# Optimization experiments

Hardware: AMD Instinct MI355X
Metric: run time of the kernel (lower is better)

Reference implementation:

```python
import jax, jax.numpy as jnp
import numpy as np

EMBED = 1024
HEADS = 16
HEAD_DIM = EMBED // HEADS
SCALE = HEAD_DIM ** -0.5


def setup_inputs() -> dict:
    key = jax.random.key(0)
    ks = jax.random.split(key, 9)
    B, N = 2, 2048
    std = EMBED ** -0.5
    return {
        "query": jax.random.normal(ks[0], (B, N, EMBED), jnp.float32),
        "key": jax.random.normal(ks[1], (B, N, EMBED), jnp.float32),
        "value": jax.random.normal(ks[2], (B, N, EMBED), jnp.float32),
        # torch nn.Linear weights are [out, in]; y = x @ W.T + b
        "Wq": jax.random.normal(ks[3], (EMBED, EMBED), jnp.float32) * std,
        "bq": jax.random.normal(ks[4], (EMBED,), jnp.float32) * 0.01,
        "Wk": jax.random.normal(ks[5], (EMBED, EMBED), jnp.float32) * std,
        "bk": jax.random.normal(ks[6], (EMBED,), jnp.float32) * 0.01,
        "Wv": jax.random.normal(ks[7], (EMBED, EMBED), jnp.float32) * std,
        "bv": jax.random.normal(ks[8], (EMBED,), jnp.float32) * 0.01,
    }


def reference(query, key, value, Wq, bq, Wk, bk, Wv, bv):
    B, NQ, _ = query.shape
    NK = key.shape[1]
    q = query @ Wq.T + bq  # [B, NQ, E]
    k = key @ Wk.T + bk    # [B, NK, E]
    v = value @ Wv.T + bv  # [B, NK, E]
    # split heads -> [B, H, N, Dh]
    q = q.reshape(B, NQ, HEADS, HEAD_DIM).transpose(0, 2, 1, 3)
    k = k.reshape(B, NK, HEADS, HEAD_DIM).transpose(0, 2, 1, 3)
    v = v.reshape(B, NK, HEADS, HEAD_DIM).transpose(0, 2, 1, 3)
    attn = jnp.einsum("bhqd,bhkd->bhqk", q, k) * SCALE  # [B, H, NQ, NK]
    attn = jax.nn.softmax(attn, axis=-1)
    out = jnp.einsum("bhqk,bhkd->bhqd", attn, v)  # [B, H, NQ, Dh]
    out = out.transpose(0, 2, 1, 3).reshape(B, NQ, EMBED)
    # o_proj is Identity (odim == embed_dim, o_proj=False); dropout is 0 (eval)
    return out
```

## Files before the change

kernel.cpp:

```cpp
#include <hip/hip_runtime.h>

#define EMB 1024
#define NSEQ 2048
#define NBATCH 2
#define NHEAD 16
#define DHEAD 64
#define QSCALE 0.18033688011112042f

typedef float f32x4 __attribute__((ext_vector_type(4)));
typedef short s16x8 __attribute__((ext_vector_type(8)));
typedef short s16x4 __attribute__((ext_vector_type(4)));

__device__ __forceinline__ short bf16r(float f) {
    unsigned u = __float_as_uint(f);
    u += 0x7fffu + ((u >> 16) & 1u);
    return (short)(u >> 16);
}

__device__ __forceinline__ unsigned pkbf(float a, float b) {
#if defined(__has_builtin) && __has_builtin(__builtin_amdgcn_cvt_pk_bf16_f32)
    auto r = __builtin_amdgcn_cvt_pk_bf16_f32(a, b);
    unsigned u;
    __builtin_memcpy(&u, &r, 4);
    return u;
#else
    return ((unsigned)bf16r(a) & 0xffffu) | ((unsigned)bf16r(b) << 16);
#endif
}

__device__ __forceinline__ float fexp2(float x) {
#if defined(__has_builtin) && __has_builtin(__builtin_amdgcn_exp2f)
    return __builtin_amdgcn_exp2f(x);
#else
    return exp2f(x);
#endif
}

__global__ __launch_bounds__(256) void proj_kernel(
    const float* __restrict__ Xq, const float* __restrict__ Xk, const float* __restrict__ Xv,
    const float* __restrict__ Wq, const float* __restrict__ Wk, const float* __restrict__ Wv,
    const float* __restrict__ bq, const float* __restrict__ bk, const float* __restrict__ bv,
    short* __restrict__ Oq, short* __restrict__ Ok, short* __restrict__ Ov)
{
    const int z = blockIdx.z;
    const float* X    = (z == 0) ? Xq : (z == 1) ? Xk : Xv;
    const float* W    = (z == 0) ? Wq : (z == 1) ? Wk : Wv;
    const float* bias = (z == 0) ? bq : (z == 1) ? bk : bv;
    short* Out        = (z == 0) ? Oq : (z == 1) ? Ok : Ov;
    const float osc   = (z == 0) ? QSCALE : 1.0f;

    const int n0 = blockIdx.x * 128;
    const int m0 = blockIdx.y * 128;

    __shared__ __align__(16) short As[128][40];
    __shared__ __align__(16) short Bs[128][40];

    const int t    = threadIdx.x;
    const int lane = t & 63;
    const int wave = t >> 6;
    const int r    = lane & 15;
    const int quad = lane >> 4;
    const int wm   = (wave >> 1) * 64;
    const int wn   = (wave & 1) * 64;

    const int srow = t >> 1;
    const int scol = (t & 1) << 4;

    f32x4 acc[4][4];
#pragma unroll
    for (int i = 0; i < 4; ++i)
#pragma unroll
        for (int j = 0; j < 4; ++j)
#pragma unroll
            for (int v = 0; v < 4; ++v) acc[i][j][v] = 0.f;

    for (int k0 = 0; k0 < EMB; k0 += 32) {
        const float4* xp = (const float4*)(X + (size_t)(m0 + srow) * EMB + k0 + scol);
        const float4* wp = (const float4*)(W + (size_t)(n0 + srow) * EMB + k0 + scol);
        float4 x0 = xp[0], x1 = xp[1], x2 = xp[2], x3 = xp[3];
        float4 w0 = wp[0], w1 = wp[1], w2 = wp[2], w3 = wp[3];
        uint4 a0 = { pkbf(x0.x, x0.y), pkbf(x0.z, x0.w), pkbf(x1.x, x1.y), pkbf(x1.z, x1.w) };
        uint4 a1 = { pkbf(x2.x, x2.y), pkbf(x2.z, x2.w), pkbf(x3.x, x3.y), pkbf(x3.z, x3.w) };
        uint4 b0 = { pkbf(w0.x, w0.y), pkbf(w0.z, w0.w), pkbf(w1.x, w1.y), pkbf(w1.z, w1.w) };
        uint4 b1 = { pkbf(w2.x, w2.y), pkbf(w2.z, w2.w), pkbf(w3.x, w3.y), pkbf(w3.z, w3.w) };
        *(uint4*)&As[srow][scol]     = a0;
        *(uint4*)&As[srow][scol + 8] = a1;
        *(uint4*)&Bs[srow][scol]     = b0;
        *(uint4*)&Bs[srow][scol + 8] = b1;
        __syncthreads();

        s16x8 af[4], bf[4];
#pragma unroll
        for (int i = 0; i < 4; ++i) af[i] = *(const s16x8*)&As[wm + i * 16 + r][quad * 8];
#pragma unroll
        for (int j = 0; j < 4; ++j) bf[j] = *(const s16x8*)&Bs[wn + j * 16 + r][quad * 8];
#pragma unroll
        for (int i = 0; i < 4; ++i)
#pragma unroll
            for (int j = 0; j < 4; ++j)
                acc[i][j] = __builtin_amdgcn_mfma_f32_16x16x32_bf16(af[i], bf[j], acc[i][j], 0, 0, 0);
        __syncthreads();
    }

#pragma unroll
    for (int j = 0; j < 4; ++j) {
        const int gn = n0 + wn + j * 16 + r;
        const float bv_ = bias[gn];
#pragma unroll
        for (int i = 0; i < 4; ++i)
#pragma unroll
            for (int reg = 0; reg < 4; ++reg) {
                const int gm = m0 + wm + i * 16 + quad * 4 + reg;
                Out[(size_t)gm * EMB + gn] = bf16r((acc[i][j][reg] + bv_) * osc);
            }
    }
}

__global__ __launch_bounds__(256) void vtrans_kernel(
    const short* __restrict__ Vp, short* __restrict__ VT)
{
    const int n0 = blockIdx.x * 64;
    const int h  = blockIdx.y;
    const int b  = blockIdx.z;
    __shared__ __align__(16) short L[64][72];

    const int t  = threadIdx.x;
    const int rr = t >> 2;
    const int cc = (t & 3) * 16;

    const short* src = Vp + (size_t)(b * NSEQ + n0 + rr) * EMB + h * DHEAD + cc;
    s16x8 a = *(const s16x8*)src;
    s16x8 c = *(const s16x8*)(src + 8);
    *(s16x8*)&L[rr][cc]     = a;
    *(s16x8*)&L[rr][cc + 8] = c;
    __syncthreads();

    const int d  = t >> 2;
    const int c4 = (t & 3) * 16;
    short vals[16];
#pragma unroll
    for (int i = 0; i < 16; ++i) vals[i] = L[c4 + i][d];
    short* dst = VT + ((size_t)(b * NHEAD + h) * DHEAD + d) * NSEQ + n0 + c4;
    *(s16x8*)dst       = *(s16x8*)&vals[0];
    *(s16x8*)(dst + 8) = *(s16x8*)&vals[8];
}

__global__ __launch_bounds__(256, 2) void attn2_kernel(
    const short* __restrict__ Qp, const short* __restrict__ Kp,
    const short* __restrict__ VT, float* __restrict__ Out)
{
    const int qblk = blockIdx.x * 128;
    const int h    = blockIdx.y;
    const int b    = blockIdx.z;

    __shared__ __align__(16) short Ks[64][72];
    __shared__ __align__(16) short Vs[64][72];
    __shared__ __align__(16) float fbuf[4][16][68];

    const int t    = threadIdx.x;
    const int lane = t & 63;
    const int w    = t >> 6;
    const int r    = lane & 15;
    const int quad = lane >> 4;

    const size_t rowbase = (size_t)b * NSEQ;
    const int colbase    = h * DHEAD;

    s16x8 qf[2][2];
#pragma unroll
    for (int qs = 0; qs < 2; ++qs)
#pragma unroll
        for (int ks = 0; ks < 2; ++ks)
            qf[qs][ks] = *(const s16x8*)(Qp + (rowbase + qblk + w * 32 + qs * 16 + r) * EMB
                                          + colbase + ks * 32 + quad * 8);

    f32x4 accO[2][4];
    float lsum[2] = {0.f, 0.f};
#pragma unroll
    for (int qs = 0; qs < 2; ++qs)
#pragma unroll
        for (int dt = 0; dt < 4; ++dt)
#pragma unroll
            for (int v = 0; v < 4; ++v) accO[qs][dt][v] = 0.f;

    const int srow = t >> 2;
    const int scol = (t & 3) << 4;

    const short* Kbase = Kp + (rowbase + srow) * EMB + colbase + scol;
    const short* Vbase = VT + ((size_t)(b * NHEAD + h) * DHEAD + srow) * NSEQ + scol;

    for (int kt = 0; kt < 32; ++kt) {
        const short* Ksrc = Kbase + (size_t)(kt * 64) * EMB;
        const short* Vsrc = Vbase + kt * 64;
        s16x8 k0 = *(const s16x8*)Ksrc, k1 = *(const s16x8*)(Ksrc + 8);
        s16x8 v0 = *(const s16x8*)Vsrc, v1 = *(const s16x8*)(Vsrc + 8);
        *(s16x8*)&Ks[srow][scol]     = k0;
        *(s16x8*)&Ks[srow][scol + 8] = k1;
        *(s16x8*)&Vs[srow][scol]     = v0;
        *(s16x8*)&Vs[srow][scol + 8] = v1;
        __syncthreads();

        s16x8 kf[4][2];
#pragma unroll
        for (int jt = 0; jt < 4; ++jt)
#pragma unroll
            for (int ks = 0; ks < 2; ++ks)
                kf[jt][ks] = *(const s16x8*)&Ks[jt * 16 + r][ks * 32 + quad * 8];

        s16x8 vf[4][2];
#pragma unroll
        for (int dt = 0; dt < 4; ++dt)
#pragma unroll
            for (int s = 0; s < 2; ++s) {
                s16x4 lo = *(const s16x4*)&Vs[dt * 16 + r][s * 32 + quad * 4];
                s16x4 hi = *(const s16x4*)&Vs[dt * 16 + r][s * 32 + 16 + quad * 4];
                vf[dt][s] = __builtin_shufflevector(lo, hi, 0, 1, 2, 3, 4, 5, 6, 7);
            }

        s16x8 pf[2][2];
#pragma unroll
        for (int qs = 0; qs < 2; ++qs) {
            f32x4 sacc[4];
#pragma unroll
            for (int jt = 0; jt < 4; ++jt) {
#pragma unroll
                for (int v = 0; v < 4; ++v) sacc[jt][v] = 0.f;
#pragma unroll
                for (int ks = 0; ks < 2; ++ks)
                    sacc[jt] = __builtin_amdgcn_mfma_f32_16x16x32_bf16(kf[jt][ks], qf[qs][ks], sacc[jt], 0, 0, 0);
            }
            float p[4][4];
#pragma unroll
            for (int jt = 0; jt < 4; ++jt)
#pragma unroll
                for (int reg = 0; reg < 4; ++reg) {
                    p[jt][reg] = fexp2(sacc[jt][reg]);
                    lsum[qs] += p[jt][reg];
                }
#pragma unroll
            for (int s = 0; s < 2; ++s) {
                uint4 uu = { pkbf(p[2 * s][0],     p[2 * s][1]),
                             pkbf(p[2 * s][2],     p[2 * s][3]),
                             pkbf(p[2 * s + 1][0], p[2 * s + 1][1]),
                             pkbf(p[2 * s + 1][2], p[2 * s + 1][3]) };
                __builtin_memcpy(&pf[qs][s], &uu, 16);
            }
        }

#pragma unroll
        for (int qs = 0; qs < 2; ++qs)
#pragma unroll
            for (int dt = 0; dt < 4; ++dt) {
                accO[qs][dt] = __builtin_amdgcn_mfma_f32_16x16x32_bf16(vf[dt][0], pf[qs][0], accO[qs][dt], 0, 0, 0);
                accO[qs][dt] = __builtin_amdgcn_mfma_f32_16x16x32_bf16(vf[dt][1], pf[qs][1], accO[qs][dt], 0, 0, 0);
            }
        __syncthreads();
    }

    float rl[2];
#pragma unroll
    for (int qs = 0; qs < 2; ++qs) {
        float s = lsum[qs];
        s += __shfl_xor(s, 16);
        s += __shfl_xor(s, 32);
        rl[qs] = 1.f / s;
    }

#pragma unroll
    for (int qs = 0; qs < 2; ++qs) {
        __syncthreads();
#pragma unroll
        for (int dt = 0; dt < 4; ++dt)
#pragma unroll
            for (int reg = 0; reg < 4; ++reg)
                fbuf[w][r][dt * 16 + quad * 4 + reg] = accO[qs][dt][reg] * rl[qs];
        __syncthreads();
        const int qi   = t >> 2;
        const int c    = (t & 3) * 16;
        const int wsrc = qi >> 4;
        const int rsrc = qi & 15;
        const float4* fp = (const float4*)&fbuf[wsrc][rsrc][c];
        float4 o0 = fp[0], o1 = fp[1], o2 = fp[2], o3 = fp[3];
        float* op = Out + (rowbase + qblk + wsrc * 32 + qs * 16 + rsrc) * EMB + colbase + c;
        ((float4*)op)[0] = o0;
        ((float4*)op)[1] = o1;
        ((float4*)op)[2] = o2;
        ((float4*)op)[3] = o3;
    }
}

__global__ __launch_bounds__(256) void attn_fb_kernel(
    const short* __restrict__ Qp, const short* __restrict__ Kp,
    const short* __restrict__ Vp, float* __restrict__ Out)
{
    const int qt = blockIdx.x;
    const int h  = blockIdx.y;
    const int b  = blockIdx.z;

    __shared__ __align__(16) short Ks[64][72];
    __shared__ __align__(16) short VsT[64][72];
    __shared__ __align__(16) short Ps[4][16][72];

    const int t    = threadIdx.x;
    const int lane = t & 63;
    const int w    = t >> 6;
    const int r    = lane & 15;
    const int quad = lane >> 4;

    const size_t rowbase = (size_t)b * NSEQ;
    const int colbase    = h * DHEAD;

    const short* Qr = Qp + (rowbase + qt * 64 + w * 16 + r) * EMB + colbase;
    const s16x8 qf0 = *(const s16x8*)(Qr + quad * 8);
    const s16x8 qf1 = *(const s16x8*)(Qr + 32 + quad * 8);

    float mrow[4], lrow[4];
    f32x4 accO[4];
#pragma unroll
    for (int i = 0; i < 4; ++i) {
        mrow[i] = -INFINITY;
        lrow[i] = 0.f;
#pragma unroll
        for (int v = 0; v < 4; ++v) accO[i][v] = 0.f;
    }

    const int srow = t >> 2;
    const int scol = (t & 3) << 4;

    for (int kt = 0; kt < 32; ++kt) {
        const short* Krow = Kp + (rowbase + kt * 64 + srow) * EMB + colbase + scol;
        const short* Vrow = Vp + (rowbase + kt * 64 + srow) * EMB + colbase + scol;
        s16x8 kv0 = *(const s16x8*)Krow;
        s16x8 kv1 = *(const s16x8*)(Krow + 8);
        s16x8 vv0 = *(const s16x8*)Vrow;
        s16x8 vv1 = *(const s16x8*)(Vrow + 8);
        *(s16x8*)&Ks[srow][scol]     = kv0;
        *(s16x8*)&Ks[srow][scol + 8] = kv1;
#pragma unroll
        for (int i = 0; i < 8; ++i) {
            VsT[scol + i][srow]     = vv0[i];
            VsT[scol + 8 + i][srow] = vv1[i];
        }
        __syncthreads();

        f32x4 sacc[4];
#pragma unroll
        for (int j = 0; j < 4; ++j) {
#pragma unroll
            for (int v = 0; v < 4; ++v) sacc[j][v] = 0.f;
            s16x8 kf0 = *(const s16x8*)&Ks[j * 16 + r][quad * 8];
            s16x8 kf1 = *(const s16x8*)&Ks[j * 16 + r][32 + quad * 8];
            sacc[j] = __builtin_amdgcn_mfma_f32_16x16x32_bf16(qf0, kf0, sacc[j], 0, 0, 0);
            sacc[j] = __builtin_amdgcn_mfma_f32_16x16x32_bf16(qf1, kf1, sacc[j], 0, 0, 0);
        }

        float rmax[4];
#pragma unroll
        for (int reg = 0; reg < 4; ++reg) rmax[reg] = -INFINITY;
#pragma unroll
        for (int j = 0; j < 4; ++j)
#pragma unroll
            for (int reg = 0; reg < 4; ++reg)
                rmax[reg] = fmaxf(rmax[reg], sacc[j][reg]);
#pragma unroll
        for (int reg = 0; reg < 4; ++reg) {
#pragma unroll
            for (int mask = 1; mask <= 8; mask <<= 1)
                rmax[reg] = fmaxf(rmax[reg], __shfl_xor(rmax[reg], mask, 64));
        }

        float alpha[4], rsum[4];
#pragma unroll
        for (int reg = 0; reg < 4; ++reg) {
            float mnew = fmaxf(mrow[reg], rmax[reg]);
            alpha[reg] = fexp2(mrow[reg] - mnew);
            mrow[reg]  = mnew;
            rsum[reg]  = 0.f;
        }

#pragma unroll
        for (int j = 0; j < 4; ++j)
#pragma unroll
            for (int reg = 0; reg < 4; ++reg) {
                float p = fexp2(sacc[j][reg] - mrow[reg]);
                rsum[reg] += p;
                Ps[w][quad * 4 + reg][j * 16 + r] = bf16r(p);
            }
#pragma unroll
        for (int reg = 0; reg < 4; ++reg) {
#pragma unroll
            for (int mask = 1; mask <= 8; mask <<= 1)
                rsum[reg] += __shfl_xor(rsum[reg], mask, 64);
            lrow[reg] = lrow[reg] * alpha[reg] + rsum[reg];
        }
#pragma unroll
        for (int j = 0; j < 4; ++j)
#pragma unroll
            for (int reg = 0; reg < 4; ++reg) accO[j][reg] *= alpha[reg];

#pragma unroll
        for (int s = 0; s < 2; ++s) {
            s16x8 pfr = *(const s16x8*)&Ps[w][r][s * 32 + quad * 8];
#pragma unroll
            for (int j = 0; j < 4; ++j) {
                s16x8 vfr = *(const s16x8*)&VsT[j * 16 + r][s * 32 + quad * 8];
                accO[j] = __builtin_amdgcn_mfma_f32_16x16x32_bf16(pfr, vfr, accO[j], 0, 0, 0);
            }
        }
        __syncthreads();
    }

#pragma unroll
    for (int j = 0; j < 4; ++j)
#pragma unroll
        for (int reg = 0; reg < 4; ++reg) {
            const int qrow = qt * 64 + w * 16 + quad * 4 + reg;
            Out[(rowbase + qrow) * EMB + colbase + j * 16 + r] = accO[j][reg] / lrow[reg];
        }
}

extern "C" void kernel_launch(void* const* d_in, const int* in_sizes, int n_in,
                              void* d_out, int out_size, void* d_ws, size_t ws_size,
                              hipStream_t stream) {
    const float* query = (const float*)d_in[0];
    const float* key   = (const float*)d_in[1];
    const float* value = (const float*)d_in[2];
    const float* Wq    = (const float*)d_in[3];
    const float* bq    = (const float*)d_in[4];
    const float* Wk    = (const float*)d_in[5];
    const float* bk    = (const float*)d_in[6];
    const float* Wv    = (const float*)d_in[7];
    const float* bv    = (const float*)d_in[8];
    float* out = (float*)d_out;

    const size_t MTOT = (size_t)NBATCH * NSEQ;
    const size_t BUF  = MTOT * EMB;
    short* Qb  = (short*)d_ws;
    short* Kb  = Qb + BUF;
    short* Vb  = Kb + BUF;
    short* VTb = Vb + BUF;

    proj_kernel<<<dim3(EMB / 128, MTOT / 128, 3), 256, 0, stream>>>(
        query, key, value, Wq, Wk, Wv, bq, bk, bv, Qb, Kb, Vb);

    if (ws_size >= 4 * BUF * sizeof(short)) {
        vtrans_kernel<<<dim3(NSEQ / 64, NHEAD, NBATCH), 256, 0, stream>>>(Vb, VTb);
        attn2_kernel<<<dim3(NSEQ / 128, NHEAD, NBATCH), 256, 0, stream>>>(Qb, Kb, VTb, out);
    } else {
        attn_fb_kernel<<<dim3(NSEQ / 64, NHEAD, NBATCH), 256, 0, stream>>>(Qb, Kb, Vb, out);
    }
}
```

Before: 235.6 us.

## Pre-convert inputs to bf16 and use direct global-to-LDS loads in projection GEMM

Adds a conversion kernel that casts the three activations and three weight matrices to bf16 in workspace. A new projection GEMM then streams these bf16 tiles straight into LDS with global_load_lds and an XOR-swizzled layout, instead of converting fp32 inside the GEMM loop. This is meant to halve GEMM operand traffic and drop in-loop conversion work. The cost is an extra full read/write pass over the inputs and a larger workspace, with the old path kept as a fallback when workspace is small.

```diff
diff --git a/kernel.cpp b/kernel.cpp
--- a/kernel.cpp
+++ b/kernel.cpp
@@ -10,6 +10,13 @@
 typedef float f32x4 __attribute__((ext_vector_type(4)));
 typedef short s16x8 __attribute__((ext_vector_type(8)));
 typedef short s16x4 __attribute__((ext_vector_type(4)));
+
+typedef __attribute__((address_space(3))) short lds_short;
+typedef __attribute__((address_space(1))) const short glb_short;
+
+__device__ __forceinline__ void gl_lds16(const short* g, short* l) {
+    __builtin_amdgcn_global_load_lds((glb_short*)g, (lds_short*)l, 16, 0, 0);
+}
 
 __device__ __forceinline__ short bf16r(float f) {
     unsigned u = __float_as_uint(f);
@@ -34,6 +41,116 @@
 #else
     return exp2f(x);
 #endif
+}
+
+__global__ __launch_bounds__(256) void cvt6_kernel(
+    const float* __restrict__ s0, const float* __restrict__ s1, const float* __restrict__ s2,
+    const float* __restrict__ s3, const float* __restrict__ s4, const float* __restrict__ s5,
+    short* __restrict__ d0, short* __restrict__ d1, short* __restrict__ d2,
+    short* __restrict__ d3, short* __restrict__ d4, short* __restrict__ d5,
+    int n0, int n1, int n2, int n3, int n4, int n5)
+{
+    const int seg = blockIdx.y;
+    const float* s = (seg == 0) ? s0 : (seg == 1) ? s1 : (seg == 2) ? s2
+                   : (seg == 3) ? s3 : (seg == 4) ? s4 : s5;
+    short* d = (seg == 0) ? d0 : (seg == 1) ? d1 : (seg == 2) ? d2
+             : (seg == 3) ? d3 : (seg == 4) ? d4 : d5;
+    const int n = (seg == 0) ? n0 : (seg == 1) ? n1 : (seg == 2) ? n2
+                : (seg == 3) ? n3 : (seg == 4) ? n4 : n5;
+
+    const int i = (blockIdx.x * 256 + threadIdx.x) * 8;
+    if (i >= n) return;
+    float4 a = *(const float4*)(s + i);
+    float4 b = *(const float4*)(s + i + 4);
+    uint4 u = { pkbf(a.x, a.y), pkbf(a.z, a.w), pkbf(b.x, b.y), pkbf(b.z, b.w) };
+    *(uint4*)(d + i) = u;
+}
+
+__global__ __launch_bounds__(256) void proj2_kernel(
+    const short* __restrict__ Xq, const short* __restrict__ Xk, const short* __restrict__ Xv,
+    const short* __restrict__ Wq, const short* __restrict__ Wk, const short* __restrict__ Wv,
+    const float* __restrict__ bq, const float* __restrict__ bk, const float* __restrict__ bv,
+    short* __restrict__ Oq, short* __restrict__ Ok, short* __restrict__ Ov)
+{
+    const int z = blockIdx.z;
+    const short* X    = (z == 0) ? Xq : (z == 1) ? Xk : Xv;
+    const short* W    = (z == 0) ? Wq : (z == 1) ? Wk : Wv;
+    const float* bias = (z == 0) ? bq : (z == 1) ? bk : bv;
+    short* Out        = (z == 0) ? Oq : (z == 1) ? Ok : Ov;
+    const float osc   = (z == 0) ? QSCALE : 1.0f;
+
+    const int n0 = blockIdx.x * 128;
+    const int m0 = blockIdx.y * 128;
+
+    __shared__ __align__(16) short As[128 * 32];
+    __shared__ __align__(16) short Bs[128 * 32];
+
+    const int t    = threadIdx.x;
+    const int lane = t & 63;
+    const int wave = t >> 6;
+    const int r    = lane & 15;
+    const int quad = lane >> 4;
+    const int wm   = (wave >> 1) * 64;
+    const int wn   = (wave & 1) * 64;
+
+    const int flat0 = t * 16;
+    const int flat1 = flat0 + 4096;
+    const int row0  = flat0 >> 6;
+    const int row1  = flat1 >> 6;
+    const int cs0   = (((flat0 >> 4) & 3) ^ (row0 & 3)) * 8;
+    const int cs1   = (((flat1 >> 4) & 3) ^ (row1 & 3)) * 8;
+
+    const short* ga0 = X + (size_t)(m0 + row0) * EMB + cs0;
+    const short* ga1 = X + (size_t)(m0 + row1) * EMB + cs1;
+    const short* gb0 = W + (size_t)(n0 + row0) * EMB + cs0;
+    const short* gb1 = W + (size_t)(n0 + row1) * EMB + cs1;
+    short* la0 = As + (flat0 >> 1);
+    short* la1 = As + (flat1 >> 1);
+    short* lb0 = Bs + (flat0 >> 1);
+    short* lb1 = Bs + (flat1 >> 1);
+
+    f32x4 acc[4][4];
+#pragma unroll
+    for (int i = 0; i < 4; ++i)
+#pragma unroll
+        for (int j = 0; j < 4; ++j)
+#pragma unroll
+            for (int v = 0; v < 4; ++v) acc[i][j][v] = 0.f;
+
+    const int fcol = (quad ^ (r & 3)) * 8;
+
+    for (int k0 = 0; k0 < EMB; k0 += 32) {
+        gl_lds16(ga0 + k0, la0);
+        gl_lds16(ga1 + k0, la1);
+        gl_lds16(gb0 + k0, lb0);
+        gl_lds16(gb1 + k0, lb1);
+        __syncthreads();
+
+        s16x8 af[4], bf[4];
+#pragma unroll
+        for (int i = 0; i < 4; ++i) af[i] = *(const s16x8*)&As[(wm + i * 16 + r) * 32 + fcol];
+#pragma unroll
+        for (int j = 0; j < 4; ++j) bf[j] = *(const s16x8*)&Bs[(wn + j * 16 + r) * 32 + fcol];
+#pragma unroll
+        for (int i = 0; i < 4; ++i)
+#pragma unroll
+            for (int j = 0; j < 4; ++j)
+                acc[i][j] = __builtin_amdgcn_mfma_f32_16x16x32_bf16(af[i], bf[j], acc[i][j], 0, 0, 0);
+        __syncthreads();
+    }
+
+#pragma unroll
+    for (int j = 0; j < 4; ++j) {
+        const int gn = n0 + wn + j * 16 + r;
+        const float bb = bias[gn];
+#pragma unroll
+        for (int i = 0; i < 4; ++i)
+#pragma unroll
+            for (int reg = 0; reg < 4; ++reg) {
+                const int gm = m0 + wm + i * 16 + quad * 4 + reg;
+                Out[(size_t)gm * EMB + gn] = bf16r((acc[i][j][reg] + bb) * osc);
+            }
+    }
 }
 
 __global__ __launch_bounds__(256) void proj_kernel(
@@ -105,13 +222,13 @@
 #pragma unroll
     for (int j = 0; j < 4; ++j) {
         const int gn = n0 + wn + j * 16 + r;
-        const float bv_ = bias[gn];
+        const float bb = bias[gn];
 #pragma unroll
         for (int i = 0; i < 4; ++i)
 #pragma unroll
             for (int reg = 0; reg < 4; ++reg) {
                 const int gm = m0 + wm + i * 16 + quad * 4 + reg;
-                Out[(size_t)gm * EMB + gn] = bf16r((acc[i][j][reg] + bv_) * osc);
+                Out[(size_t)gm * EMB + gn] = bf16r((acc[i][j][reg] + bb) * osc);
             }
     }
 }
@@ -433,20 +550,40 @@
     const float* bv    = (const float*)d_in[8];
     float* out = (float*)d_out;
 
-    const size_t MTOT = (size_t)NBATCH * NSEQ;
-    const size_t BUF  = MTOT * EMB;
+    const size_t XBUF = (size_t)NBATCH * NSEQ * EMB;
+    const size_t WBUF = (size_t)EMB * EMB;
+
     short* Qb  = (short*)d_ws;
-    short* Kb  = Qb + BUF;
-    short* Vb  = Kb + BUF;
-    short* VTb = Vb + BUF;
-
-    proj_kernel<<<dim3(EMB / 128, MTOT / 128, 3), 256, 0, stream>>>(
-        query, key, value, Wq, Wk, Wv, bq, bk, bv, Qb, Kb, Vb);
-
-    if (ws_size >= 4 * BUF * sizeof(short)) {
+    short* Kb  = Qb + XBUF;
+    short* Vb  = Kb + XBUF;
+    short* VTb = Vb + XBUF;
+    short* Xqb = VTb + XBUF;
+    short* Xkb = Xqb + XBUF;
+    short* Xvb = Xkb + XBUF;
+    short* Wqb = Xvb + XBUF;
+    short* Wkb = Wqb + WBUF;
+    short* Wvb = Wkb + WBUF;
+
+    const size_t need_full  = (7 * XBUF + 3 * WBUF) * sizeof(short);
+    const size_t need_attn2 = 4 * XBUF * sizeof(short);
+
+    if (ws_size >= need_full) {
+        cvt6_kernel<<<dim3(2048, 6), 256, 0, stream>>>(
+            query, key, value, Wq, Wk, Wv,
+            Xqb, Xkb, Xvb, Wqb, Wkb, Wvb,
+            (int)XBUF, (int)XBUF, (int)XBUF, (int)WBUF, (int)WBUF, (int)WBUF);
+        proj2_kernel<<<dim3(EMB / 128, (NBATCH * NSEQ) / 128, 3), 256, 0, stream>>>(
+            Xqb, Xkb, Xvb, Wqb, Wkb, Wvb, bq, bk, bv, Qb, Kb, Vb);
+        vtrans_kernel<<<dim3(NSEQ / 64, NHEAD, NBATCH), 256, 0, stream>>>(Vb, VTb);
+        attn2_kernel<<<dim3(NSEQ / 128, NHEAD, NBATCH), 256, 0, stream>>>(Qb, Kb, VTb, out);
+    } else if (ws_size >= need_attn2) {
+        proj_kernel<<<dim3(EMB / 128, (NBATCH * NSEQ) / 128, 3), 256, 0, stream>>>(
+            query, key, value, Wq, Wk, Wv, bq, bk, bv, Qb, Kb, Vb);
         vtrans_kernel<<<dim3(NSEQ / 64, NHEAD, NBATCH), 256, 0, stream>>>(Vb, VTb);
         attn2_kernel<<<dim3(NSEQ / 128, NHEAD, NBATCH), 256, 0, stream>>>(Qb, Kb, VTb, out);
     } else {
+        proj_kernel<<<dim3(EMB / 128, (NBATCH * NSEQ) / 128, 3), 256, 0, stream>>>(
+            query, key, value, Wq, Wk, Wv, bq, bk, bv, Qb, Kb, Vb);
         attn_fb_kernel<<<dim3(NSEQ / 64, NHEAD, NBATCH), 256, 0, stream>>>(Qb, Kb, Vb, out);
     }
 }
```

After: 207.2 us. -12.1%, faster.
